# Optimization experiments

Measured on AMD Instinct MI355X. Metric: run time of the kernel, lower is better.

## Reference

```python
import jax, jax.numpy as jnp
import numpy as np

TEMPERATURE = 0.1
NORM_EPS = 1e-12          # F.normalize default eps
SMALL_VAL = float(np.finfo(np.float32).tiny)  # pytorch-metric-learning small_val(float32)
NEG_INF = float(np.finfo(np.float32).min)     # c_f.neg_inf for masked logsumexp


def setup_inputs() -> dict:
    key = jax.random.key(0)
    k1, k2 = jax.random.split(key)
    N, D = 8192, 128
    emb = jax.random.normal(k1, (N, D), dtype=jnp.float32)
    labels = jax.random.randint(k2, (N,), 0, 1000, dtype=jnp.int64)
    return {"emb": emb, "labels": labels}


def reference(emb, labels):
    N = emb.shape[0]
    # F.normalize(emb, dim=1): x / max(||x||, eps)
    norms = jnp.linalg.norm(emb, axis=1, keepdims=True)
    x = emb / jnp.maximum(norms, NORM_EPS)

    # cosine similarity matrix [N, N], scaled by temperature
    mat = jnp.matmul(x, x.T) / TEMPERATURE

    same = labels[:, None] == labels[None, :]
    diag = jnp.eye(N, dtype=bool)
    pos_mask = same & ~diag          # same label, i != j
    keep_mask = ~diag                # pos + neg (all off-diagonal)

    # numerical stability: subtract detached row max (over full row, incl. diagonal)
    mat_max = jax.lax.stop_gradient(jnp.max(mat, axis=1, keepdims=True))
    mat = mat - mat_max

    # masked logsumexp over off-diagonal entries
    masked = jnp.where(keep_mask, mat, NEG_INF)
    denom = jax.nn.logsumexp(masked, axis=1, keepdims=True)  # [N, 1]

    log_prob = mat - denom
    pos_f = pos_mask.astype(mat.dtype)
    mean_log_prob_pos = jnp.sum(pos_f * log_prob, axis=1) / (
        jnp.sum(pos_f, axis=1) + SMALL_VAL
    )
    losses = -mean_log_prob_pos  # per-element losses
    # SumReducer: sum over elements
    return jnp.sum(losses)
```

## Files before the change

### kernel.cpp

```cpp
#include <hip/hip_runtime.h>
#include <hip/hip_bf16.h>


typedef __bf16 bf16_t;
typedef __bf16 bf16x2 __attribute__((ext_vector_type(2)));
typedef __bf16 bf16x8 __attribute__((ext_vector_type(8)));
typedef float f32x16 __attribute__((ext_vector_type(16)));

#define NN 8192
#define DIM 128
#define MAIN_BLOCKS 2080
#define SMALL_VAL 1.17549435e-38f
#define L2E10 14.4269504089f
#define LN2 0.69314718056f

__device__ inline size_t swz(int row, int lane) {
    int f = lane >> 3, hh = (lane >> 2) & 1, j = (lane & 3) << 1;
    return ((size_t)(row >> 5) * 4096) + f * 512 + hh * 256 + (row & 31) * 8 + j;
}

#define DPPADD(v, ctrl, rmask)                                                         \
    do {                                                                               \
        int _t = __builtin_amdgcn_update_dpp(0, __float_as_int((v)), (ctrl), (rmask),  \
                                             0xf, true);                               \
        (v) += __int_as_float(_t);                                                     \
    } while (0)

__device__ inline float half32_sum(float v) {
    DPPADD(v, 0x111, 0xf);
    DPPADD(v, 0x112, 0xf);
    DPPADD(v, 0x114, 0xf);
    DPPADD(v, 0x118, 0xf);
    DPPADD(v, 0x142, 0xa);
    return v;
}

__device__ inline void gload_lds16(const bf16_t* g, bf16_t* l) {
    __builtin_amdgcn_global_load_lds(
        (const __attribute__((address_space(1))) unsigned int*)g,
        (__attribute__((address_space(3))) unsigned int*)l, 16, 0, 0);
}

__global__ __launch_bounds__(256) void norm_csum(const float* __restrict__ emb,
                                                 const int* __restrict__ labels,
                                                 bf16_t* __restrict__ xsw,
                                                 float* __restrict__ cd_arr,
                                                 float* __restrict__ sd_arr,
                                                 float* __restrict__ cm1_arr,
                                                 float* __restrict__ se_acc,
                                                 float* __restrict__ out) {
    __shared__ float cs[DIM];
    __shared__ int rowlist[96];
    __shared__ int nrows;
    int cls = blockIdx.x;
    int wv = threadIdx.x >> 6, lane = threadIdx.x & 63;
    if (threadIdx.x < DIM) cs[threadIdx.x] = 0.f;
    if (threadIdx.x == 0) nrows = 0;
    if (threadIdx.x < 8) se_acc[cls * 8 + threadIdx.x] = 0.f;
    if (cls == 0 && threadIdx.x == 0) *out = 0.f;
    __syncthreads();

    float s0 = 0.f, s1 = 0.f;
    const int4* lab4 = (const int4*)(labels + wv * 2048);
#pragma unroll
    for (int it = 0; it < 8; ++it) {
        int4 l = lab4[it * 64 + lane];
        int base = wv * 2048 + it * 256;
#pragma unroll
        for (int cmp = 0; cmp < 4; ++cmp) {
            int li = (cmp == 0) ? l.x : (cmp == 1) ? l.y : (cmp == 2) ? l.z : l.w;
            unsigned long long m = __ballot(li == cls);
            while (m) {
                int bb = __builtin_ctzll(m);
                m &= m - 1;
                int row = base + 4 * bb + cmp;
                float2 v = ((const float2*)emb)[row * 64 + lane];
                float ss = fmaf(v.x, v.x, v.y * v.y);
#pragma unroll
                for (int mm = 1; mm < 64; mm <<= 1) ss += __shfl_xor(ss, mm, 64);
                float inv = 1.0f / fmaxf(sqrtf(ss), 1e-12f);
                bf16x2 o; o.x = (bf16_t)(v.x * inv); o.y = (bf16_t)(v.y * inv);
                *(bf16x2*)(xsw + swz(row, lane)) = o;
                s0 += (float)o.x; s1 += (float)o.y;
                if (lane == 0) {
                    int idx = atomicAdd(&nrows, 1);
                    if (idx < 96) rowlist[idx] = row;
                }
            }
        }
    }
    atomicAdd(&cs[2 * lane], s0);
    atomicAdd(&cs[2 * lane + 1], s1);
    __syncthreads();
    int n = nrows;
    for (int k = wv; k < n; k += 4) {
        int row = rowlist[k];
        bf16x2 xv = *(const bf16x2*)(xsw + swz(row, lane));
        float x0 = (float)xv.x, x1 = (float)xv.y;
        float cdp = fmaf(x0, cs[2 * lane], x1 * cs[2 * lane + 1]);
        float sdp = fmaf(x0, x0, x1 * x1);
#pragma unroll
        for (int mm = 1; mm < 64; mm <<= 1) {
            cdp += __shfl_xor(cdp, mm, 64);
            sdp += __shfl_xor(sdp, mm, 64);
        }
        if (lane == 0) {
            cd_arr[row] = cdp; sd_arr[row] = sdp; cm1_arr[row] = (float)(n - 1);
        }
    }
}

__global__ __launch_bounds__(256, 5) void supcon_main(const bf16_t* __restrict__ xsw,
                                                      float* __restrict__ se_acc) {
    __shared__ bf16_t bst[4 * 4096];

    int b = blockIdx.x;
    int cq = (int)((sqrtf(8.f * (float)b + 1.f) - 1.f) * 0.5f);
    while ((cq + 1) * (cq + 2) / 2 <= b) ++cq;
    while (cq * (cq + 1) / 2 > b) --cq;
    int g = b - cq * (cq + 1) / 2;

    int wv = threadIdx.x >> 6, lane = threadIdx.x & 63;
    int I = 4 * g + wv;
    int c = lane & 31, h = lane >> 5;
    int laneoff = h * 256 + c * 8;

    const bf16_t* abase = xsw + (size_t)I * 4096 + laneoff;
    bf16x8 a[8];
#pragma unroll
    for (int f = 0; f < 8; ++f) a[f] = *(const bf16x8*)(abase + f * 512);

    {
        const bf16_t* gsrc = xsw + (size_t)cq * 4 * 4096;
#pragma unroll
        for (int i = 0; i < 8; ++i) {
            int k = i * 4 + wv;
            gload_lds16(gsrc + k * 512 + lane * 8, bst + k * 512);
        }
    }
    __syncthreads();

    float se[16];
#pragma unroll
    for (int r = 0; r < 16; ++r) se[r] = 0.f;

    bf16x8 cur[8], nxt[8];
#pragma unroll
    for (int f = 0; f < 8; ++f) cur[f] = *(const bf16x8*)(bst + laneoff + f * 512);

#pragma unroll
    for (int t = 0; t < 4; ++t) {
        if (t < 3) {
            const bf16_t* btn = bst + (t + 1) * 4096 + laneoff;
#pragma unroll
            for (int f = 0; f < 8; ++f) nxt[f] = *(const bf16x8*)(btn + f * 512);
        }
        f32x16 acc0, acc1;
#pragma unroll
        for (int r = 0; r < 16; ++r) { acc0[r] = 0.f; acc1[r] = 0.f; }
#pragma unroll
        for (int f = 0; f < 8; f += 2) {
            acc0 = __builtin_amdgcn_mfma_f32_32x32x16_bf16(a[f], cur[f], acc0, 0, 0, 0);
            acc1 = __builtin_amdgcn_mfma_f32_32x32x16_bf16(a[f + 1], cur[f + 1], acc1, 0, 0, 0);
        }
        int ct = cq * 4 + t;
        if (ct >= I) {
            float c0 = 0.f, c1 = 0.f, c2 = 0.f, c3 = 0.f;
#pragma unroll
            for (int r = 0; r < 16; ++r) {
                float s = acc0[r] + acc1[r];
                float e = __builtin_amdgcn_exp2f(fmaf(s, L2E10, -L2E10));
                se[r] += e;
                if ((r & 3) == 0) c0 += e; else if ((r & 3) == 1) c1 += e;
                else if ((r & 3) == 2) c2 += e; else c3 += e;
            }
            if (ct > I) {
                float v = (c0 + c1) + (c2 + c3);
                v += __shfl_xor(v, 32, 64);
                if (h == 0) atomicAdd(&se_acc[ct * 32 + c], v);
            }
        }
        if (t < 3) {
#pragma unroll
            for (int f = 0; f < 8; ++f) cur[f] = nxt[f];
        }
    }

#pragma unroll
    for (int r = 0; r < 16; ++r) se[r] = half32_sum(se[r]);
    if (c == 31) {
        int rowbase = I * 32 + 4 * h;
#pragma unroll
        for (int r = 0; r < 16; ++r)
            atomicAdd(&se_acc[rowbase + (r & 3) + 8 * (r >> 2)], se[r]);
    }
}

__global__ __launch_bounds__(256) void finalize_kernel(const float* __restrict__ se_acc,
                                                       const float* __restrict__ cd_arr,
                                                       const float* __restrict__ sd_arr,
                                                       const float* __restrict__ cm1_arr,
                                                       float* __restrict__ out) {
    __shared__ float part[4];
    int i = blockIdx.x * 256 + threadIdx.x;
    float sd = sd_arr[i], cd = cd_arr[i], cm1 = cm1_arr[i];
    float diag = __builtin_amdgcn_exp2f(fmaf(sd, L2E10, -L2E10));
    float sev  = fmaxf(se_acc[i] - diag, 1e-30f);
    float lse  = fmaf(__builtin_amdgcn_logf(sev), LN2, 10.f);
    float loss = (cm1 * lse - 10.f * (cd - sd)) / (cm1 + SMALL_VAL);
#pragma unroll
    for (int m = 1; m < 64; m <<= 1) loss += __shfl_xor(loss, m, 64);
    int wv = threadIdx.x >> 6;
    if ((threadIdx.x & 63) == 0) part[wv] = loss;
    __syncthreads();
    if (threadIdx.x == 0) atomicAdd(out, part[0] + part[1] + part[2] + part[3]);
}

extern "C" void kernel_launch(void* const* d_in, const int* in_sizes, int n_in,
                              void* d_out, int out_size, void* d_ws, size_t ws_size,
                              hipStream_t stream) {
    const float* emb  = (const float*)d_in[0];
    const int* labels = (const int*)d_in[1];

    char* ws = (char*)d_ws;
    bf16_t* xsw = (bf16_t*)ws;
    float* se   = (float*)(ws + (size_t)NN * DIM * 2);
    float* cd   = se + NN;
    float* sd   = cd + NN;
    float* cm1  = sd + NN;

    norm_csum<<<1024, 256, 0, stream>>>(emb, labels, xsw, cd, sd, cm1, se, (float*)d_out);
    supcon_main<<<MAIN_BLOCKS, 256, 0, stream>>>(xsw, se);
    finalize_kernel<<<NN / 256, 256, 0, stream>>>(se, cd, sd, cm1, (float*)d_out);
}
```

Before: 112.6 us.

## Replace triangular atomic similarity kernel with full-sweep partial sums

The symmetric triangular tiling, which accumulated row and column exp-sums with global atomics, is replaced by a full N×N sweep. Each wave now owns 64 rows and iterates over 16 column-group partitions, using double-buffered LDS loads of B tiles. Each block writes per-sweep partial row sums to a buffer that the finalize kernel reduces, so the zero-init and atomics go away. In exchange it doubles the MFMA and exp work by no longer exploiting symmetry, and it launches far fewer, heavier blocks.

```diff
diff --git a/kernel.cpp b/kernel.cpp
--- a/kernel.cpp
+++ b/kernel.cpp
@@ -9,7 +9,7 @@
 
 #define NN 8192
 #define DIM 128
-#define MAIN_BLOCKS 2080
+#define SWEEP 16
 #define SMALL_VAL 1.17549435e-38f
 #define L2E10 14.4269504089f
 #define LN2 0.69314718056f
@@ -47,7 +47,6 @@
                                                  float* __restrict__ cd_arr,
                                                  float* __restrict__ sd_arr,
                                                  float* __restrict__ cm1_arr,
-                                                 float* __restrict__ se_acc,
                                                  float* __restrict__ out) {
     __shared__ float cs[DIM];
     __shared__ int rowlist[96];
@@ -56,7 +55,6 @@
     int wv = threadIdx.x >> 6, lane = threadIdx.x & 63;
     if (threadIdx.x < DIM) cs[threadIdx.x] = 0.f;
     if (threadIdx.x == 0) nrows = 0;
-    if (threadIdx.x < 8) se_acc[cls * 8 + threadIdx.x] = 0.f;
     if (cls == 0 && threadIdx.x == 0) *out = 0.f;
     __syncthreads();
 
@@ -110,102 +108,111 @@
     }
 }
 
-__global__ __launch_bounds__(256, 5) void supcon_main(const bf16_t* __restrict__ xsw,
-                                                      float* __restrict__ se_acc) {
-    __shared__ bf16_t bst[4 * 4096];
-
-    int b = blockIdx.x;
-    int cq = (int)((sqrtf(8.f * (float)b + 1.f) - 1.f) * 0.5f);
-    while ((cq + 1) * (cq + 2) / 2 <= b) ++cq;
-    while (cq * (cq + 1) / 2 > b) --cq;
-    int g = b - cq * (cq + 1) / 2;
-
+__global__ __launch_bounds__(256, 2) void supcon_sweep(const bf16_t* __restrict__ xsw,
+                                                       float* __restrict__ se_part) {
+    __shared__ bf16_t bst[2][4 * 4096];
+
+    int s = blockIdx.x & 15, bg = blockIdx.x >> 4;
     int wv = threadIdx.x >> 6, lane = threadIdx.x & 63;
-    int I = 4 * g + wv;
+    int bnd = bg * 4 + wv;
     int c = lane & 31, h = lane >> 5;
     int laneoff = h * 256 + c * 8;
 
-    const bf16_t* abase = xsw + (size_t)I * 4096 + laneoff;
-    bf16x8 a[8];
-#pragma unroll
-    for (int f = 0; f < 8; ++f) a[f] = *(const bf16x8*)(abase + f * 512);
+    const bf16_t* alo = xsw + (size_t)(bnd * 2) * 4096 + laneoff;
+    bf16x8 a_lo[8], a_hi[8];
+#pragma unroll
+    for (int f = 0; f < 8; ++f) {
+        a_lo[f] = *(const bf16x8*)(alo + f * 512);
+        a_hi[f] = *(const bf16x8*)(alo + 4096 + f * 512);
+    }
+
+    float se_lo[16], se_hi[16];
+#pragma unroll
+    for (int r = 0; r < 16; ++r) { se_lo[r] = 0.f; se_hi[r] = 0.f; }
 
     {
-        const bf16_t* gsrc = xsw + (size_t)cq * 4 * 4096;
+        const bf16_t* gsrc = xsw + (size_t)s * 4 * 4096;
 #pragma unroll
         for (int i = 0; i < 8; ++i) {
-            int k = i * 4 + wv;
-            gload_lds16(gsrc + k * 512 + lane * 8, bst + k * 512);
-        }
-    }
-    __syncthreads();
-
-    float se[16];
-#pragma unroll
-    for (int r = 0; r < 16; ++r) se[r] = 0.f;
-
-    bf16x8 cur[8], nxt[8];
-#pragma unroll
-    for (int f = 0; f < 8; ++f) cur[f] = *(const bf16x8*)(bst + laneoff + f * 512);
-
-#pragma unroll
-    for (int t = 0; t < 4; ++t) {
-        if (t < 3) {
-            const bf16_t* btn = bst + (t + 1) * 4096 + laneoff;
-#pragma unroll
-            for (int f = 0; f < 8; ++f) nxt[f] = *(const bf16x8*)(btn + f * 512);
-        }
-        f32x16 acc0, acc1;
-#pragma unroll
-        for (int r = 0; r < 16; ++r) { acc0[r] = 0.f; acc1[r] = 0.f; }
-#pragma unroll
-        for (int f = 0; f < 8; f += 2) {
-            acc0 = __builtin_amdgcn_mfma_f32_32x32x16_bf16(a[f], cur[f], acc0, 0, 0, 0);
-            acc1 = __builtin_amdgcn_mfma_f32_32x32x16_bf16(a[f + 1], cur[f + 1], acc1, 0, 0, 0);
-        }
-        int ct = cq * 4 + t;
-        if (ct >= I) {
-            float c0 = 0.f, c1 = 0.f, c2 = 0.f, c3 = 0.f;
+            int kk = i * 4 + wv;
+            gload_lds16(gsrc + kk * 512 + lane * 8, &bst[0][kk * 512]);
+        }
+    }
+    __syncthreads();
+
+#pragma unroll
+    for (int k = 0; k < 4; ++k) {
+        if (k < 3) {
+            const bf16_t* gsrc = xsw + (size_t)(s + 16 * (k + 1)) * 4 * 4096;
+            bf16_t* dbuf = &bst[(k + 1) & 1][0];
+#pragma unroll
+            for (int i = 0; i < 8; ++i) {
+                int kk = i * 4 + wv;
+                gload_lds16(gsrc + kk * 512 + lane * 8, dbuf + kk * 512);
+            }
+        }
+        const bf16_t* bb = &bst[k & 1][0];
+
+        bf16x8 cur[8], nxt[8];
+#pragma unroll
+        for (int f = 0; f < 8; ++f) cur[f] = *(const bf16x8*)(bb + laneoff + f * 512);
+#pragma unroll
+        for (int t = 0; t < 4; ++t) {
+            if (t < 3) {
+                const bf16_t* btn = bb + (t + 1) * 4096 + laneoff;
+#pragma unroll
+                for (int f = 0; f < 8; ++f) nxt[f] = *(const bf16x8*)(btn + f * 512);
+            }
+            f32x16 acclo, acchi;
+#pragma unroll
+            for (int r = 0; r < 16; ++r) { acclo[r] = 0.f; acchi[r] = 0.f; }
+#pragma unroll
+            for (int f = 0; f < 8; ++f) {
+                acclo = __builtin_amdgcn_mfma_f32_32x32x16_bf16(a_lo[f], cur[f], acclo, 0, 0, 0);
+                acchi = __builtin_amdgcn_mfma_f32_32x32x16_bf16(a_hi[f], cur[f], acchi, 0, 0, 0);
+            }
 #pragma unroll
             for (int r = 0; r < 16; ++r) {
-                float s = acc0[r] + acc1[r];
-                float e = __builtin_amdgcn_exp2f(fmaf(s, L2E10, -L2E10));
-                se[r] += e;
-                if ((r & 3) == 0) c0 += e; else if ((r & 3) == 1) c1 += e;
-                else if ((r & 3) == 2) c2 += e; else c3 += e;
-            }
-            if (ct > I) {
-                float v = (c0 + c1) + (c2 + c3);
-                v += __shfl_xor(v, 32, 64);
-                if (h == 0) atomicAdd(&se_acc[ct * 32 + c], v);
-            }
-        }
-        if (t < 3) {
-#pragma unroll
-            for (int f = 0; f < 8; ++f) cur[f] = nxt[f];
-        }
-    }
-
-#pragma unroll
-    for (int r = 0; r < 16; ++r) se[r] = half32_sum(se[r]);
+                se_lo[r] += __builtin_amdgcn_exp2f(fmaf(acclo[r], L2E10, -L2E10));
+                se_hi[r] += __builtin_amdgcn_exp2f(fmaf(acchi[r], L2E10, -L2E10));
+            }
+            if (t < 3) {
+#pragma unroll
+                for (int f = 0; f < 8; ++f) cur[f] = nxt[f];
+            }
+        }
+        __syncthreads();
+    }
+
+#pragma unroll
+    for (int r = 0; r < 16; ++r) {
+        se_lo[r] = half32_sum(se_lo[r]);
+        se_hi[r] = half32_sum(se_hi[r]);
+    }
     if (c == 31) {
-        int rowbase = I * 32 + 4 * h;
-#pragma unroll
-        for (int r = 0; r < 16; ++r)
-            atomicAdd(&se_acc[rowbase + (r & 3) + 8 * (r >> 2)], se[r]);
-    }
-}
-
-__global__ __launch_bounds__(256) void finalize_kernel(const float* __restrict__ se_acc,
+        float* dst = se_part + (size_t)s * NN + bnd * 64 + 4 * h;
+#pragma unroll
+        for (int r = 0; r < 16; ++r) {
+            int ro = (r & 3) + 8 * (r >> 2);
+            dst[ro]      = se_lo[r];
+            dst[32 + ro] = se_hi[r];
+        }
+    }
+}
+
+__global__ __launch_bounds__(256) void finalize_kernel(const float* __restrict__ se_part,
                                                        const float* __restrict__ cd_arr,
                                                        const float* __restrict__ sd_arr,
                                                        const float* __restrict__ cm1_arr,
                                                        float* __restrict__ out) {
     __shared__ float part[4];
     int i = blockIdx.x * 256 + threadIdx.x;
+    float sev_raw = 0.f;
+#pragma unroll
+    for (int s = 0; s < SWEEP; ++s) sev_raw += se_part[(size_t)s * NN + i];
     float sd = sd_arr[i], cd = cd_arr[i], cm1 = cm1_arr[i];
     float diag = __builtin_amdgcn_exp2f(fmaf(sd, L2E10, -L2E10));
-    float sev  = fmaxf(se_acc[i] - diag, 1e-30f);
+    float sev  = fmaxf(sev_raw - diag, 1e-30f);
     float lse  = fmaf(__builtin_amdgcn_logf(sev), LN2, 10.f);
     float loss = (cm1 * lse - 10.f * (cd - sd)) / (cm1 + SMALL_VAL);
 #pragma unroll
@@ -223,13 +230,13 @@
     const int* labels = (const int*)d_in[1];
 
     char* ws = (char*)d_ws;
-    bf16_t* xsw = (bf16_t*)ws;
-    float* se   = (float*)(ws + (size_t)NN * DIM * 2);
-    float* cd   = se + NN;
-    float* sd   = cd + NN;
-    float* cm1  = sd + NN;
-
-    norm_csum<<<1024, 256, 0, stream>>>(emb, labels, xsw, cd, sd, cm1, se, (float*)d_out);
-    supcon_main<<<MAIN_BLOCKS, 256, 0, stream>>>(xsw, se);
-    finalize_kernel<<<NN / 256, 256, 0, stream>>>(se, cd, sd, cm1, (float*)d_out);
-}
+    bf16_t* xsw   = (bf16_t*)ws;
+    float* separt = (float*)(ws + (size_t)NN * DIM * 2);
+    float* cd     = separt + (size_t)SWEEP * NN;
+    float* sd     = cd + NN;
+    float* cm1    = sd + NN;
+
+    norm_csum<<<1024, 256, 0, stream>>>(emb, labels, xsw, cd, sd, cm1, (float*)d_out);
+    supcon_sweep<<<512, 256, 0, stream>>>(xsw, separt);
+    finalize_kernel<<<NN / 256, 256, 0, stream>>>(separt, cd, sd, cm1, (float*)d_out);
+}
```

Result: slower. 135.4 us (+20.2%).
